# Kernel tuning notes

Hardware: AMD Instinct MI355X
Metric: run time of the kernel (lower is better)

## Reference

```python
import jax, jax.numpy as jnp
import numpy as np

NUM_GRAPHS = 256
NEG_SLOPE = 0.2


def _gatv2(x, src, dst, Wl, Wr, att, bias, num_nodes):
    # GATv2Conv (heads=1): e_ij = att . leaky_relu(Wl x_j + Wr x_i), softmax over in-edges of i
    xl = x @ Wl  # [N, H] source transform
    xr = x @ Wr  # [N, H] target transform
    msg = xl[src]                      # [E, H]
    e = jax.nn.leaky_relu(msg + xr[dst], NEG_SLOPE) @ att  # [E]
    # segment softmax over destination node
    e_max = jax.ops.segment_max(e, dst, num_segments=num_nodes)
    e_exp = jnp.exp(e - e_max[dst])
    denom = jax.ops.segment_sum(e_exp, dst, num_segments=num_nodes)
    alpha = e_exp / denom[dst]         # [E]
    out = jax.ops.segment_sum(alpha[:, None] * msg, dst, num_segments=num_nodes)
    return out + bias


def setup_inputs() -> dict:
    key = jax.random.key(0)
    ks = jax.random.split(key, 16)
    N, E, D, H, O = 100000, 1600000, 64, 64, 64
    s = 0.05
    inp = {
        "x": jax.random.normal(ks[0], (N, D), dtype=jnp.float32),
        "edge_index": jax.random.randint(ks[1], (2, E), 0, N, dtype=jnp.int64),
        "batch": jnp.sort(jax.random.randint(ks[2], (N,), 0, NUM_GRAPHS, dtype=jnp.int64)),
        "W1l": jax.random.normal(ks[3], (D, H), dtype=jnp.float32) * s,
        "W1r": jax.random.normal(ks[4], (D, H), dtype=jnp.float32) * s,
        "att1": jax.random.normal(ks[5], (H,), dtype=jnp.float32) * s,
        "b1": jnp.zeros((H,), dtype=jnp.float32),
        "W2": jax.random.normal(ks[6], (H, H), dtype=jnp.float32) * s,
        "att2": jax.random.normal(ks[7], (H,), dtype=jnp.float32) * s,
        "b2": jnp.zeros((H,), dtype=jnp.float32),
        "W3": jax.random.normal(ks[8], (H, H), dtype=jnp.float32) * s,
        "att3": jax.random.normal(ks[9], (H,), dtype=jnp.float32) * s,
        "b3": jnp.zeros((H,), dtype=jnp.float32),
        "Wlin": jax.random.normal(ks[10], (H, O), dtype=jnp.float32) * s,
        "blin": jnp.zeros((O,), dtype=jnp.float32),
    }
    return inp


def reference(x, edge_index, batch, W1l, W1r, att1, b1, W2, att2, b2, W3, att3, b3, Wlin, blin):
    N = x.shape[0]
    # PyG GATv2Conv default add_self_loops=True
    loops = jnp.arange(N, dtype=edge_index.dtype)
    src = jnp.concatenate([edge_index[0], loops])
    dst = jnp.concatenate([edge_index[1], loops])

    h = jax.nn.relu(_gatv2(x, src, dst, W1l, W1r, att1, b1, N))
    h = jax.nn.relu(_gatv2(h, src, dst, W2, W2, att2, b2, N))  # share_weights=True
    h = _gatv2(h, src, dst, W3, W3, att3, b3, N)

    # global mean pool over graphs
    sums = jax.ops.segment_sum(h, batch, num_segments=NUM_GRAPHS)
    cnts = jax.ops.segment_sum(jnp.ones((N,), dtype=h.dtype), batch, num_segments=NUM_GRAPHS)
    pooled = sums / jnp.maximum(cnts, 1.0)[:, None]
    # dropout is identity in eval mode
    return pooled @ Wlin + blin
```

## Files before the change

kernel.cpp:

```cpp
#include <hip/hip_runtime.h>
#include <hip/hip_fp16.h>
#include <math.h>

#define NEG_SLOPE 0.2f
#define NUM_GRAPHS 256
#define LOG2E_F 1.44269504088896f

#define EPB   6656
#define EPT   13
#define BCAP  5120
#define MAXB  392

typedef _Float16 half8 __attribute__((ext_vector_type(8)));
typedef _Float16 f16x2 __attribute__((ext_vector_type(2)));
typedef float f32x4 __attribute__((ext_vector_type(4)));

__device__ __forceinline__ half8 bch8(uint4 u) { return __builtin_bit_cast(half8, u); }
__device__ __forceinline__ f16x2 bc2(unsigned u) { return __builtin_bit_cast(f16x2, u); }

__device__ __forceinline__ float hsum8_bcast(float x) {
    x += __int_as_float(__builtin_amdgcn_update_dpp(0, __float_as_int(x), 0x111, 0xF, 0xF, false));
    x += __int_as_float(__builtin_amdgcn_update_dpp(0, __float_as_int(x), 0x112, 0xF, 0xF, false));
    x += __int_as_float(__builtin_amdgcn_update_dpp(0, __float_as_int(x), 0x114, 0xF, 0xF, false));
    return __int_as_float(__builtin_amdgcn_ds_swizzle(__float_as_int(x), 0xF8));
}


__device__ __forceinline__ void bucketA_body(char* smem, int bid, int t,
                                             const int* __restrict__ src,
                                             const int* __restrict__ dst,
                                             unsigned* __restrict__ bucketFill,
                                             uint2* __restrict__ bucketArr,
                                             int E, int NBUCK) {
    uint2* sEdge = (uint2*)smem;
    unsigned* hist  = (unsigned*)(smem + EPB * 8);
    unsigned* lscan = hist + MAXB;
    unsigned* ebase = lscan + MAXB;
    unsigned* efill = ebase + MAXB;
    int e0 = bid * EPB;
    int cntE = E - e0; if (cntE > EPB) cntE = EPB;

    for (int b = t; b < MAXB; b += 512) { hist[b] = 0u; efill[b] = 0u; }
    __syncthreads();

    int es[EPT], ed[EPT];
#pragma unroll
    for (int k = 0; k < EPT; ++k) {
        int i = t + k * 512;
        bool v = i < cntE;
        es[k] = v ? src[e0 + i] : 0;
        ed[k] = v ? dst[e0 + i] : -1;
        if (v) atomicAdd(&hist[(unsigned)ed[k] >> 8], 1u);
    }
    __syncthreads();

    if (t < 64) {
        unsigned vals[7]; unsigned tot = 0u;
#pragma unroll
        for (int k = 0; k < 7; ++k) {
            int b = t * 7 + k;
            vals[k] = (b < MAXB) ? hist[b] : 0u;
            tot += vals[k];
        }
        unsigned sc = tot;
#pragma unroll
        for (int off = 1; off < 64; off <<= 1) {
            unsigned n = __shfl_up(sc, off, 64);
            if (t >= off) sc += n;
        }
        unsigned run = sc - tot;
#pragma unroll
        for (int k = 0; k < 7; ++k) {
            int b = t * 7 + k;
            if (b < MAXB) { lscan[b] = run; run += vals[k]; }
        }
    }
    __syncthreads();

    for (int b = t; b < NBUCK; b += 512) {
        unsigned c = hist[b];
        ebase[b] = c ? atomicAdd(&bucketFill[b], c) : 0u;
    }
    __syncthreads();

#pragma unroll
    for (int k = 0; k < EPT; ++k) {
        if (ed[k] >= 0) {
            unsigned b = (unsigned)ed[k] >> 8;
            unsigned p = lscan[b] + atomicAdd(&efill[b], 1u);
            sEdge[p] = make_uint2((unsigned)es[k], (unsigned)ed[k]);
        }
    }
    __syncthreads();

    for (int i = t; i < cntE; i += 512) {
        uint2 e = sEdge[i];
        unsigned b = e.y >> 8;
        unsigned pos = ebase[b] + ((unsigned)i - lscan[b]);
        if (pos < BCAP) bucketArr[(size_t)b * BCAP + pos] = e;
    }
}


__device__ __forceinline__ void stage_x32_row(const float* __restrict__ X, _Float16* sXp,
                                              int r0, int lr, int c0, int N) {
    int row = r0 + lr;
    float4 x0, x1, x2, x3;
    if (row < N) {
        const float4* Xv = (const float4*)(X + (size_t)row * 64 + c0);
        x0 = Xv[0]; x1 = Xv[1]; x2 = Xv[2]; x3 = Xv[3];
    } else {
        x0 = x1 = x2 = x3 = make_float4(0.f, 0.f, 0.f, 0.f);
    }
    __half2 hh[8] = {
        __floats2half2_rn(x0.x, x0.y), __floats2half2_rn(x0.z, x0.w),
        __floats2half2_rn(x1.x, x1.y), __floats2half2_rn(x1.z, x1.w),
        __floats2half2_rn(x2.x, x2.y), __floats2half2_rn(x2.z, x2.w),
        __floats2half2_rn(x3.x, x3.y), __floats2half2_rn(x3.z, x3.w)};
    *(uint4*)(sXp + lr * 72 + c0)     = ((uint4*)hh)[0];
    *(uint4*)(sXp + lr * 72 + c0 + 8) = ((uint4*)hh)[1];
}

__device__ __forceinline__ void stage_x16(const __half* __restrict__ X, _Float16* sXp,
                                          int r0, int t, int N) {
    int lr = t >> 2, c0 = (t & 3) * 16;
    int row = r0 + lr;
    uint4 u0 = make_uint4(0u,0u,0u,0u), u1 = u0;
    if (row < N) {
        const uint4* Xv = (const uint4*)(X + (size_t)row * 64 + c0);
        u0 = Xv[0]; u1 = Xv[1];
    }
    *(uint4*)(sXp + lr * 72 + c0)     = u0;
    *(uint4*)(sXp + lr * 72 + c0 + 8) = u1;
}

__device__ __forceinline__ void stage_wt(const float* __restrict__ W, _Float16* sWt, int t) {
    int k = t >> 2, nq = (t & 3) * 16;
    const float4* wr = (const float4*)(W + k * 64 + nq);
    float4 w0 = wr[0], w1 = wr[1], w2 = wr[2], w3 = wr[3];
    float ws[16] = {w0.x, w0.y, w0.z, w0.w, w1.x, w1.y, w1.z, w1.w,
                    w2.x, w2.y, w2.z, w2.w, w3.x, w3.y, w3.z, w3.w};
#pragma unroll
    for (int i = 0; i < 16; ++i)
        sWt[(nq + i) * 72 + k] = (_Float16)ws[i];
}

__device__ __forceinline__ void stage_wt512(const float* __restrict__ W, _Float16* sWt, int t) {
    int k = t >> 3, nq = (t & 7) * 8;
    const float4* wr = (const float4*)(W + k * 64 + nq);
    float4 w0 = wr[0], w1 = wr[1];
    float ws[8] = {w0.x, w0.y, w0.z, w0.w, w1.x, w1.y, w1.z, w1.w};
#pragma unroll
    for (int i = 0; i < 8; ++i)
        sWt[(nq + i) * 72 + k] = (_Float16)ws[i];
}

__device__ __forceinline__ void mfma_tile(const _Float16* sXp, const _Float16* sWt,
                                          int m0, int lane, f32x4 acc[4]) {
    int lrow = lane & 15, hi = lane >> 4;
    uint4 ua0 = *(const uint4*)(sXp + (m0 + lrow) * 72 + hi * 8);
    uint4 ua1 = *(const uint4*)(sXp + (m0 + lrow) * 72 + 32 + hi * 8);
    half8 a0 = bch8(ua0), a1 = bch8(ua1);
#pragma unroll
    for (int nt = 0; nt < 4; ++nt) {
        uint4 ub0 = *(const uint4*)(sWt + (nt * 16 + lrow) * 72 + hi * 8);
        uint4 ub1 = *(const uint4*)(sWt + (nt * 16 + lrow) * 72 + 32 + hi * 8);
        acc[nt] = __builtin_amdgcn_mfma_f32_16x16x32_f16(a0, bch8(ub0), acc[nt], 0, 0, 0);
        acc[nt] = __builtin_amdgcn_mfma_f32_16x16x32_f16(a1, bch8(ub1), acc[nt], 0, 0, 0);
    }
}

__device__ __forceinline__ void mfma_store_co(const f32x4 acc[4], __half* Y16,
                                              _Float16* srow, int r0, int m0,
                                              int lane, int N) {
    int lrow = lane & 15, hi = lane >> 4;
#pragma unroll
    for (int nt = 0; nt < 4; ++nt)
#pragma unroll
        for (int r = 0; r < 4; ++r)
            srow[(hi * 4 + r) * 72 + nt * 16 + lrow] = (_Float16)acc[nt][r];
    __syncthreads();
    int row = lane >> 3, c8 = (lane & 7) * 8;
#pragma unroll
    for (int i = 0; i < 2; ++i) {
        int m = r0 + m0 + row + i * 8;
        uint4 v = *(const uint4*)(srow + (row + i * 8) * 72 + c8);
        if (m < N) *(uint4*)(Y16 + (size_t)m * 64 + c8) = v;
    }
}

__global__ __launch_bounds__(512) void k_gemm1_bucketA(
        const float* __restrict__ X, const float* __restrict__ Wl, const float* __restrict__ Wr,
        __half* __restrict__ Yl16, __half* __restrict__ Yr16, int N,
        const int* __restrict__ src, const int* __restrict__ dst,
        unsigned* __restrict__ bucketFill, uint2* __restrict__ bucketArr,
        int E, int NBUCK, int aBlocks, int g1Blocks,
        const float* __restrict__ att1, const float* __restrict__ att2,
        const float* __restrict__ att3, __half* __restrict__ att16) {
    __shared__ uint4 smemq[3720];
    char* smem = (char*)smemq;
    int bid = blockIdx.x;
    int t = threadIdx.x;
    if (bid < aBlocks) {
        bucketA_body(smem, bid, t, src, dst, bucketFill, bucketArr, E, NBUCK);
        return;
    }
    if (bid >= aBlocks + g1Blocks) {
        if (t < 192) {
            int layer = t >> 6, f = t & 63;
            const float* ap = (layer == 0) ? att1 : (layer == 1) ? att2 : att3;
            att16[layer * 64 + f] = __float2half(ap[f] * LOG2E_F);
        }
        return;
    }
    _Float16* sXp  = (_Float16*)smem;
    _Float16* sWtl = sXp + 128 * 72;
    _Float16* sWtr = sWtl + 64 * 72;
    _Float16* srep = sWtr + 64 * 72;
    int r0 = (bid - aBlocks) * 128;
    stage_x32_row(X, sXp, r0, t >> 2, (t & 3) * 16, N);
    stage_wt512(Wl, sWtl, t);
    stage_wt512(Wr, sWtr, t);
    __syncthreads();
    int lane = t & 63;
    int m0 = (t >> 6) * 16;
    _Float16* srow = srep + (t >> 6) * 16 * 72;
    f32x4 accl[4] = {}, accr[4] = {};
    mfma_tile(sXp, sWtl, m0, lane, accl);
    mfma_tile(sXp, sWtr, m0, lane, accr);
    mfma_store_co(accl, Yl16, srow, r0, m0, lane, N);
    mfma_store_co(accr, Yr16, srow, r0, m0, lane, N);
}

__global__ __launch_bounds__(512) void k_bucketB(const uint2* __restrict__ bucketArr,
                                                 const unsigned* __restrict__ bucketFill,
                                                 int* __restrict__ cnt, int* __restrict__ csrF,
                                                 const int* __restrict__ batch,
                                                 int* __restrict__ gstart,
                                                 int N, int E) {
    __shared__ int stage[256 * 64];
    __shared__ unsigned h[256];
    int t = threadIdx.x;
    int b = blockIdx.x;
    int n0 = b << 8;
    if (t < 256) h[t] = 1u;
    {
        uint4* sz = (uint4*)stage;
#pragma unroll
        for (int k = 0; k < 8; ++k) sz[t + k * 512] = make_uint4(0u, 0u, 0u, 0u);
    }
    __syncthreads();
    if (t < 256) stage[t << 6] = n0 + t;
    __syncthreads();

    unsigned ec = bucketFill[b]; if (ec > BCAP) ec = BCAP;
    for (unsigned i = t; i < ec; i += 512) {
        uint2 e = bucketArr[(size_t)b * BCAP + i];
        unsigned v = e.y & 255u;
        unsigned r = atomicAdd(&h[v], 1u);
        if (r < 64u) {
            unsigned pos = (r < 32u) ? (((r & 7u) << 2) + (r >> 3))
                                     : (32u + ((r & 7u) << 2) + ((r >> 3) - 4u));
            stage[(v << 6) + pos] = (int)e.x;
        }
    }
    __syncthreads();

    int node = n0 + t;
    if (t < 256 && node < N) {
        unsigned d = h[t];
        cnt[node] = (int)(d < 64u ? d : 64u);
        int bb = batch[node];
        if (node == 0) {
            for (int g = 0; g <= bb; ++g) gstart[g] = 0;
        } else {
            int pb = batch[node - 1];
            for (int g = pb + 1; g <= bb; ++g) gstart[g] = node;
        }
        if (node == N - 1) {
            for (int g = bb + 1; g <= NUM_GRAPHS; ++g) gstart[g] = N;
        }
    }

    int nrows = N - n0; if (nrows > 256) nrows = 256;
    int total4 = nrows << 4;
    uint4* d4 = (uint4*)(csrF + ((size_t)n0 << 6));
    const uint4* s4 = (const uint4*)stage;
    for (int k = t; k < total4; k += 512) d4[k] = s4[k];
}

__global__ __launch_bounds__(256) void k_gemm_l2(const __half* __restrict__ X,
                                                 const float* __restrict__ W,
                                                 __half* __restrict__ Y16, int N) {
    __shared__ _Float16 s[64 * 72 + 64 * 72 + 4 * 16 * 72];
    _Float16* sXp = s;
    _Float16* sWt = s + 64 * 72;
    _Float16* srep = sWt + 64 * 72;
    int t = threadIdx.x;
    int r0 = blockIdx.x * 64;
    stage_x16(X, sXp, r0, t, N);
    stage_wt(W, sWt, t);
    __syncthreads();
    int lane = t & 63;
    int m0 = (t >> 6) * 16;
    _Float16* srow = srep + (t >> 6) * 16 * 72;
    f32x4 acc[4] = {};
    mfma_tile(sXp, sWt, m0, lane, acc);
    mfma_store_co(acc, Y16, srow, r0, m0, lane, N);
}


#define AGG_STEP(P, K)                                                       \
    { half8 v_ = bch8(P);                                                    \
      half8 t_ = v_ + X8;                                                    \
      t_ = __builtin_elementwise_max(t_, t_ * (_Float16)NEG_SLOPE);          \
      uint4 tu_ = __builtin_bit_cast(uint4, t_);                             \
      float sc_ = __builtin_amdgcn_fdot2(bc2(ua.x), bc2(tu_.x), 0.f, false); \
      sc_ = __builtin_amdgcn_fdot2(bc2(ua.y), bc2(tu_.y), sc_, false);       \
      sc_ = __builtin_amdgcn_fdot2(bc2(ua.z), bc2(tu_.z), sc_, false);       \
      sc_ = __builtin_amdgcn_fdot2(bc2(ua.w), bc2(tu_.w), sc_, false);       \
      sc_ = hsum8_bcast(sc_);                                                \
      float w_ = ((K) * 8 + s < degs) ? exp2f(sc_) : 0.f;                    \
      l_acc += w_;                                                           \
      _Pragma("unroll") for (int j_ = 0; j_ < 8; ++j_)                       \
          acc[j_] = fmaf((float)v_[j_], w_, acc[j_]);                        \
    }

__global__ void k_agg8(const __half* __restrict__ xl, const __half* __restrict__ xrh,
                       const __half* __restrict__ att16, const float* __restrict__ bias,
                       const int* __restrict__ cnt, const int* __restrict__ csrF,
                       float* __restrict__ out32, __half* __restrict__ out16,
                       int N, int do_relu) {
    int wid = (blockIdx.x * blockDim.x + threadIdx.x) >> 6;
    if (wid >= N) return;
    int lane = threadIdx.x & 63;
    int q = lane & 7, s = lane >> 3;
    int fb = q * 8;

    int degs = __builtin_amdgcn_readfirstlane(cnt[wid]);
    const int* crow = csrF + ((size_t)wid << 6);

    uint4 idx = *(const uint4*)(crow + s * 4);
    uint4 ux = *(const uint4*)(xrh + ((size_t)wid << 6) + fb);
    uint4 ua = *(const uint4*)(att16 + fb);

    uint4 pA = *(const uint4*)(xl + ((size_t)idx.x << 6) + fb);
    uint4 pB = *(const uint4*)(xl + ((size_t)idx.y << 6) + fb);
    uint4 pC = *(const uint4*)(xl + ((size_t)idx.z << 6) + fb);
    uint4 pD = *(const uint4*)(xl + ((size_t)idx.w << 6) + fb);

    half8 X8 = bch8(ux);
    float l_acc = 0.f;
    float acc[8];
#pragma unroll
    for (int j = 0; j < 8; ++j) acc[j] = 0.f;

    AGG_STEP(pA, 0);
    if (degs > 8)  AGG_STEP(pB, 1);
    if (degs > 16) AGG_STEP(pC, 2);
    if (degs > 24) {
        AGG_STEP(pD, 3);
        if (degs > 32) {
            uint4 idx2 = *(const uint4*)(crow + 32 + s * 4);
            uint4 qA = *(const uint4*)(xl + ((size_t)idx2.x << 6) + fb);
            uint4 qB = *(const uint4*)(xl + ((size_t)idx2.y << 6) + fb);
            uint4 qC = *(const uint4*)(xl + ((size_t)idx2.z << 6) + fb);
            uint4 qD = *(const uint4*)(xl + ((size_t)idx2.w << 6) + fb);
            AGG_STEP(qA, 4);
            if (degs > 40) AGG_STEP(qB, 5);
            if (degs > 48) AGG_STEP(qC, 6);
            if (degs > 56) AGG_STEP(qD, 7);
        }
    }

#pragma unroll
    for (int o = 8; o <= 32; o <<= 1) {
        l_acc += __shfl_xor(l_acc, o, 64);
#pragma unroll
        for (int j = 0; j < 8; ++j) acc[j] += __shfl_xor(acc[j], o, 64);
    }

    if (s < 2) {
        float rl = 1.0f / l_acc;
        float a0 = s ? acc[4] : acc[0];
        float a1 = s ? acc[5] : acc[1];
        float a2 = s ? acc[6] : acc[2];
        float a3 = s ? acc[7] : acc[3];
        int fo = fb + s * 4;
        float4 bv = *(const float4*)(bias + fo);
        a0 = a0 * rl + bv.x; a1 = a1 * rl + bv.y;
        a2 = a2 * rl + bv.z; a3 = a3 * rl + bv.w;
        if (do_relu) {
            a0 = fmaxf(a0, 0.f); a1 = fmaxf(a1, 0.f);
            a2 = fmaxf(a2, 0.f); a3 = fmaxf(a3, 0.f);
        }
        if (out16) {
            __half2 h0 = __floats2half2_rn(a0, a1);
            __half2 h1 = __floats2half2_rn(a2, a3);
            uint2 u;
            u.x = __builtin_bit_cast(unsigned, h0);
            u.y = __builtin_bit_cast(unsigned, h1);
            *(uint2*)(out16 + (size_t)wid * 64 + fo) = u;
        } else {
            *(float4*)(out32 + (size_t)wid * 64 + fo) = make_float4(a0, a1, a2, a3);
        }
    }
}


__global__ __launch_bounds__(256) void k_pool_final(const __half* __restrict__ h16,
                                                    const int* __restrict__ gstart,
                                                    const float* __restrict__ Wlin,
                                                    const float* __restrict__ blin,
                                                    float* __restrict__ out) {
    __shared__ float red[4][64];
    int g = blockIdx.x;
    int t = threadIdx.x;
    int w = t >> 6, lane = t & 63;
    int i0 = gstart[g], i1 = gstart[g + 1];
    const unsigned* hu = (const unsigned*)h16;
    int half_ = lane >> 5;
    int u = lane & 31;
    float sx = 0.f, sy = 0.f;
    for (int i = i0 + w * 2 + half_; i < i1; i += 8) {
        unsigned v = hu[(size_t)i * 32 + u];
        float2 p = __half22float2(__builtin_bit_cast(__half2, v));
        sx += p.x; sy += p.y;
    }
    sx += __shfl_xor(sx, 32, 64);
    sy += __shfl_xor(sy, 32, 64);
    if (lane < 32) { red[w][2 * u] = sx; red[w][2 * u + 1] = sy; }
    __syncthreads();
    if (w == 0) {
        float s = red[0][lane] + red[1][lane] + red[2][lane] + red[3][lane];
        float cden = (float)((i1 - i0) > 1 ? (i1 - i0) : 1);
        float pld = s / cden;
        float acc = blin[lane];
        for (int k = 0; k < 64; ++k) {
            acc += __shfl(pld, k, 64) * Wlin[k * 64 + lane];
        }
        out[g * 64 + lane] = acc;
    }
}


extern "C" void kernel_launch(void* const* d_in, const int* in_sizes, int n_in,
                              void* d_out, int out_size, void* d_ws, size_t ws_size,
                              hipStream_t stream) {
    const float* x    = (const float*)d_in[0];
    const int*   ei   = (const int*)d_in[1];
    const int*   batch= (const int*)d_in[2];
    const float* W1l  = (const float*)d_in[3];
    const float* W1r  = (const float*)d_in[4];
    const float* att1 = (const float*)d_in[5];
    const float* b1   = (const float*)d_in[6];
    const float* W2   = (const float*)d_in[7];
    const float* att2 = (const float*)d_in[8];
    const float* b2   = (const float*)d_in[9];
    const float* W3   = (const float*)d_in[10];
    const float* att3 = (const float*)d_in[11];
    const float* b3   = (const float*)d_in[12];
    const float* Wlin = (const float*)d_in[13];
    const float* blin = (const float*)d_in[14];

    const int N = in_sizes[0] / 64;
    const int E = in_sizes[1] / 2;
    const int* src = ei;
    const int* dst = ei + E;
    const int NBUCK = (N + 255) >> 8;

    char* p = (char*)d_ws;
    auto alloc = [&](size_t bytes) -> void* {
        void* r = (void*)p;
        p += (bytes + 255) & ~(size_t)255;
        return r;
    };
    float*  bufB32 = (float*)alloc((size_t)N * 64 * 4);
    __half* buf16  = (__half*)alloc((size_t)N * 64 * 2);
    __half* bufC16 = (__half*)alloc((size_t)N * 64 * 2);
    int*    csrF   = (int*)alloc((size_t)N * 64 * 4);
    int*    cnt    = (int*)alloc((size_t)N * 4);
    int*    gstart = (int*)alloc((size_t)(NUM_GRAPHS + 1) * 4);
    __half* att16  = (__half*)alloc((size_t)3 * 64 * 2);
    uint2*    bucketArr  = (uint2*)bufB32;
    unsigned* bucketFill = (unsigned*)((char*)bufB32 + ((size_t)20 << 20));

    const int B = 256;
    const int gemmBlocks = (N + 63) / 64;
    const int aggBlocks = ((size_t)N * 64 + B - 1) / B;
    const int aBlocks = (E + EPB - 1) / EPB;
    const int g1Blocks = (N + 127) >> 7;

    hipMemsetAsync(bucketFill, 0, (size_t)NBUCK * 4, stream);
    k_gemm1_bucketA<<<aBlocks + g1Blocks + 1, 512, 0, stream>>>(
        x, W1l, W1r, buf16, bufC16, N, src, dst, bucketFill, bucketArr,
        E, NBUCK, aBlocks, g1Blocks, att1, att2, att3, att16);
    k_bucketB<<<NBUCK, 512, 0, stream>>>(bucketArr, bucketFill, cnt, csrF, batch, gstart, N, E);

    k_agg8<<<aggBlocks, B, 0, stream>>>(buf16, bufC16, att16, b1, cnt, csrF,
                                        nullptr, bufC16, N, 1);
    k_gemm_l2<<<gemmBlocks, B, 0, stream>>>(bufC16, W2, buf16, N);
    k_agg8<<<aggBlocks, B, 0, stream>>>(buf16, buf16, att16 + 64, b2, cnt, csrF,
                                        nullptr, bufC16, N, 1);
    k_gemm_l2<<<gemmBlocks, B, 0, stream>>>(bufC16, W3, buf16, N);
    k_agg8<<<aggBlocks, B, 0, stream>>>(buf16, buf16, att16 + 128, b3, cnt, csrF,
                                        nullptr, bufC16, N, 0);

    k_pool_final<<<NUM_GRAPHS, B, 0, stream>>>(bufC16, gstart, Wlin, blin, (float*)d_out);
}
```

Before: 293.3 us.

## Use nontemporal loads/stores, 128-row GEMM tiles, and trimmed agg reduction

```diff
diff --git a/kernel.cpp b/kernel.cpp
--- a/kernel.cpp
+++ b/kernel.cpp
@@ -14,8 +14,11 @@
 typedef _Float16 half8 __attribute__((ext_vector_type(8)));
 typedef _Float16 f16x2 __attribute__((ext_vector_type(2)));
 typedef float f32x4 __attribute__((ext_vector_type(4)));
+typedef unsigned u32x2 __attribute__((ext_vector_type(2)));
+typedef unsigned u32x4 __attribute__((ext_vector_type(4)));
 
 __device__ __forceinline__ half8 bch8(uint4 u) { return __builtin_bit_cast(half8, u); }
+__device__ __forceinline__ half8 bch8v(u32x4 u) { return __builtin_bit_cast(half8, u); }
 __device__ __forceinline__ f16x2 bc2(unsigned u) { return __builtin_bit_cast(f16x2, u); }
 
 __device__ __forceinline__ float hsum8_bcast(float x) {
@@ -48,8 +51,8 @@
     for (int k = 0; k < EPT; ++k) {
         int i = t + k * 512;
         bool v = i < cntE;
-        es[k] = v ? src[e0 + i] : 0;
-        ed[k] = v ? dst[e0 + i] : -1;
+        es[k] = v ? __builtin_nontemporal_load(src + e0 + i) : 0;
+        ed[k] = v ? __builtin_nontemporal_load(dst + e0 + i) : -1;
         if (v) atomicAdd(&hist[(unsigned)ed[k] >> 8], 1u);
     }
     __syncthreads();
@@ -97,7 +100,10 @@
         uint2 e = sEdge[i];
         unsigned b = e.y >> 8;
         unsigned pos = ebase[b] + ((unsigned)i - lscan[b]);
-        if (pos < BCAP) bucketArr[(size_t)b * BCAP + pos] = e;
+        if (pos < BCAP) {
+            u32x2 pe; pe[0] = e.x; pe[1] = e.y;
+            __builtin_nontemporal_store(pe, (u32x2*)&bucketArr[(size_t)b * BCAP + pos]);
+        }
     }
 }
 
@@ -105,18 +111,19 @@
 __device__ __forceinline__ void stage_x32_row(const float* __restrict__ X, _Float16* sXp,
                                               int r0, int lr, int c0, int N) {
     int row = r0 + lr;
-    float4 x0, x1, x2, x3;
+    f32x4 x0 = {0.f,0.f,0.f,0.f}, x1 = x0, x2 = x0, x3 = x0;
     if (row < N) {
-        const float4* Xv = (const float4*)(X + (size_t)row * 64 + c0);
-        x0 = Xv[0]; x1 = Xv[1]; x2 = Xv[2]; x3 = Xv[3];
-    } else {
-        x0 = x1 = x2 = x3 = make_float4(0.f, 0.f, 0.f, 0.f);
+        const f32x4* Xv = (const f32x4*)(X + (size_t)row * 64 + c0);
+        x0 = __builtin_nontemporal_load(Xv);
+        x1 = __builtin_nontemporal_load(Xv + 1);
+        x2 = __builtin_nontemporal_load(Xv + 2);
+        x3 = __builtin_nontemporal_load(Xv + 3);
     }
     __half2 hh[8] = {
-        __floats2half2_rn(x0.x, x0.y), __floats2half2_rn(x0.z, x0.w),
-        __floats2half2_rn(x1.x, x1.y), __floats2half2_rn(x1.z, x1.w),
-        __floats2half2_rn(x2.x, x2.y), __floats2half2_rn(x2.z, x2.w),
-        __floats2half2_rn(x3.x, x3.y), __floats2half2_rn(x3.z, x3.w)};
+        __floats2half2_rn(x0[0], x0[1]), __floats2half2_rn(x0[2], x0[3]),
+        __floats2half2_rn(x1[0], x1[1]), __floats2half2_rn(x1[2], x1[3]),
+        __floats2half2_rn(x2[0], x2[1]), __floats2half2_rn(x2[2], x2[3]),
+        __floats2half2_rn(x3[0], x3[1]), __floats2half2_rn(x3[2], x3[3])};
     *(uint4*)(sXp + lr * 72 + c0)     = ((uint4*)hh)[0];
     *(uint4*)(sXp + lr * 72 + c0 + 8) = ((uint4*)hh)[1];
 }
@@ -125,13 +132,14 @@
                                           int r0, int t, int N) {
     int lr = t >> 2, c0 = (t & 3) * 16;
     int row = r0 + lr;
-    uint4 u0 = make_uint4(0u,0u,0u,0u), u1 = u0;
+    u32x4 u0 = {0u,0u,0u,0u}, u1 = u0;
     if (row < N) {
-        const uint4* Xv = (const uint4*)(X + (size_t)row * 64 + c0);
-        u0 = Xv[0]; u1 = Xv[1];
-    }
-    *(uint4*)(sXp + lr * 72 + c0)     = u0;
-    *(uint4*)(sXp + lr * 72 + c0 + 8) = u1;
+        const u32x4* Xv = (const u32x4*)(X + (size_t)row * 64 + c0);
+        u0 = __builtin_nontemporal_load(Xv);
+        u1 = __builtin_nontemporal_load(Xv + 1);
+    }
+    *(u32x4*)(sXp + lr * 72 + c0)     = u0;
+    *(u32x4*)(sXp + lr * 72 + c0 + 8) = u1;
 }
 
 __device__ __forceinline__ void stage_wt(const float* __restrict__ W, _Float16* sWt, int t) {
@@ -255,13 +263,13 @@
 
     unsigned ec = bucketFill[b]; if (ec > BCAP) ec = BCAP;
     for (unsigned i = t; i < ec; i += 512) {
-        uint2 e = bucketArr[(size_t)b * BCAP + i];
-        unsigned v = e.y & 255u;
+        u32x2 e = __builtin_nontemporal_load((const u32x2*)&bucketArr[(size_t)b * BCAP + i]);
+        unsigned v = e[1] & 255u;
         unsigned r = atomicAdd(&h[v], 1u);
         if (r < 64u) {
             unsigned pos = (r < 32u) ? (((r & 7u) << 2) + (r >> 3))
                                      : (32u + ((r & 7u) << 2) + ((r >> 3) - 4u));
-            stage[(v << 6) + pos] = (int)e.x;
+            stage[(v << 6) + pos] = (int)e[0];
         }
     }
     __syncthreads();
@@ -292,21 +300,26 @@
 __global__ __launch_bounds__(256) void k_gemm_l2(const __half* __restrict__ X,
                                                  const float* __restrict__ W,
                                                  __half* __restrict__ Y16, int N) {
-    __shared__ _Float16 s[64 * 72 + 64 * 72 + 4 * 16 * 72];
+    __shared__ _Float16 s[128 * 72 + 64 * 72 + 4 * 16 * 72];
     _Float16* sXp = s;
-    _Float16* sWt = s + 64 * 72;
+    _Float16* sWt = s + 128 * 72;
     _Float16* srep = sWt + 64 * 72;
     int t = threadIdx.x;
-    int r0 = blockIdx.x * 64;
+    int r0 = blockIdx.x * 128;
     stage_x16(X, sXp, r0, t, N);
+    stage_x16(X, sXp + 64 * 72, r0 + 64, t, N);
     stage_wt(W, sWt, t);
     __syncthreads();
     int lane = t & 63;
-    int m0 = (t >> 6) * 16;
-    _Float16* srow = srep + (t >> 6) * 16 * 72;
-    f32x4 acc[4] = {};
-    mfma_tile(sXp, sWt, m0, lane, acc);
-    mfma_store_co(acc, Y16, srow, r0, m0, lane, N);
+    int w = t >> 6;
+    _Float16* srow = srep + w * 16 * 72;
+#pragma unroll
+    for (int half_ = 0; half_ < 2; ++half_) {
+        int m0 = half_ * 64 + w * 16;
+        f32x4 acc[4] = {};
+        mfma_tile(sXp, sWt, m0, lane, acc);
+        mfma_store_co(acc, Y16, srow, r0, m0, lane, N);
+    }
 }
 
 
@@ -329,8 +342,7 @@
 __global__ void k_agg8(const __half* __restrict__ xl, const __half* __restrict__ xrh,
                        const __half* __restrict__ att16, const float* __restrict__ bias,
                        const int* __restrict__ cnt, const int* __restrict__ csrF,
-                       float* __restrict__ out32, __half* __restrict__ out16,
-                       int N, int do_relu) {
+                       __half* __restrict__ out16, int N, int do_relu) {
     int wid = (blockIdx.x * blockDim.x + threadIdx.x) >> 6;
     if (wid >= N) return;
     int lane = threadIdx.x & 63;
@@ -340,14 +352,14 @@
     int degs = __builtin_amdgcn_readfirstlane(cnt[wid]);
     const int* crow = csrF + ((size_t)wid << 6);
 
-    uint4 idx = *(const uint4*)(crow + s * 4);
+    u32x4 idxv = __builtin_nontemporal_load((const u32x4*)(crow + s * 4));
     uint4 ux = *(const uint4*)(xrh + ((size_t)wid << 6) + fb);
     uint4 ua = *(const uint4*)(att16 + fb);
 
-    uint4 pA = *(const uint4*)(xl + ((size_t)idx.x << 6) + fb);
-    uint4 pB = *(const uint4*)(xl + ((size_t)idx.y << 6) + fb);
-    uint4 pC = *(const uint4*)(xl + ((size_t)idx.z << 6) + fb);
-    uint4 pD = *(const uint4*)(xl + ((size_t)idx.w << 6) + fb);
+    uint4 pA = *(const uint4*)(xl + ((size_t)idxv[0] << 6) + fb);
+    uint4 pB = *(const uint4*)(xl + ((size_t)idxv[1] << 6) + fb);
+    uint4 pC = *(const uint4*)(xl + ((size_t)idxv[2] << 6) + fb);
+    uint4 pD = *(const uint4*)(xl + ((size_t)idxv[3] << 6) + fb);
 
     half8 X8 = bch8(ux);
     float l_acc = 0.f;
@@ -361,11 +373,11 @@
     if (degs > 24) {
         AGG_STEP(pD, 3);
         if (degs > 32) {
-            uint4 idx2 = *(const uint4*)(crow + 32 + s * 4);
-            uint4 qA = *(const uint4*)(xl + ((size_t)idx2.x << 6) + fb);
-            uint4 qB = *(const uint4*)(xl + ((size_t)idx2.y << 6) + fb);
-            uint4 qC = *(const uint4*)(xl + ((size_t)idx2.z << 6) + fb);
-            uint4 qD = *(const uint4*)(xl + ((size_t)idx2.w << 6) + fb);
+            u32x4 idx2 = __builtin_nontemporal_load((const u32x4*)(crow + 32 + s * 4));
+            uint4 qA = *(const uint4*)(xl + ((size_t)idx2[0] << 6) + fb);
+            uint4 qB = *(const uint4*)(xl + ((size_t)idx2[1] << 6) + fb);
+            uint4 qC = *(const uint4*)(xl + ((size_t)idx2[2] << 6) + fb);
+            uint4 qD = *(const uint4*)(xl + ((size_t)idx2[3] << 6) + fb);
             AGG_STEP(qA, 4);
             if (degs > 40) AGG_STEP(qB, 5);
             if (degs > 48) AGG_STEP(qC, 6);
@@ -373,37 +385,41 @@
         }
     }
 
-#pragma unroll
-    for (int o = 8; o <= 32; o <<= 1) {
+    l_acc += __shfl_xor(l_acc, 8, 64);
+#pragma unroll
+    for (int j = 0; j < 8; ++j) acc[j] += __shfl_xor(acc[j], 8, 64);
+    int par = s & 1;
+    float b0 = par ? acc[4] : acc[0];
+    float b1 = par ? acc[5] : acc[1];
+    float b2 = par ? acc[6] : acc[2];
+    float b3 = par ? acc[7] : acc[3];
+#pragma unroll
+    for (int o = 16; o <= 32; o <<= 1) {
         l_acc += __shfl_xor(l_acc, o, 64);
-#pragma unroll
-        for (int j = 0; j < 8; ++j) acc[j] += __shfl_xor(acc[j], o, 64);
+        b0 += __shfl_xor(b0, o, 64);
+        b1 += __shfl_xor(b1, o, 64);
+        b2 += __shfl_xor(b2, o, 64);
+        b3 += __shfl_xor(b3, o, 64);
     }
 
     if (s < 2) {
         float rl = 1.0f / l_acc;
-        float a0 = s ? acc[4] : acc[0];
-        float a1 = s ? acc[5] : acc[1];
-        float a2 = s ? acc[6] : acc[2];
-        float a3 = s ? acc[7] : acc[3];
         int fo = fb + s * 4;
         float4 bv = *(const float4*)(bias + fo);
-        a0 = a0 * rl + bv.x; a1 = a1 * rl + bv.y;
-        a2 = a2 * rl + bv.z; a3 = a3 * rl + bv.w;
+        float a0 = b0 * rl + bv.x;
+        float a1 = b1 * rl + bv.y;
+        float a2 = b2 * rl + bv.z;
+        float a3 = b3 * rl + bv.w;
         if (do_relu) {
             a0 = fmaxf(a0, 0.f); a1 = fmaxf(a1, 0.f);
             a2 = fmaxf(a2, 0.f); a3 = fmaxf(a3, 0.f);
         }
-        if (out16) {
-            __half2 h0 = __floats2half2_rn(a0, a1);
-            __half2 h1 = __floats2half2_rn(a2, a3);
-            uint2 u;
-            u.x = __builtin_bit_cast(unsigned, h0);
-            u.y = __builtin_bit_cast(unsigned, h1);
-            *(uint2*)(out16 + (size_t)wid * 64 + fo) = u;
-        } else {
-            *(float4*)(out32 + (size_t)wid * 64 + fo) = make_float4(a0, a1, a2, a3);
-        }
+        __half2 h0 = __floats2half2_rn(a0, a1);
+        __half2 h1 = __floats2half2_rn(a2, a3);
+        u32x2 u;
+        u[0] = __builtin_bit_cast(unsigned, h0);
+        u[1] = __builtin_bit_cast(unsigned, h1);
+        __builtin_nontemporal_store(u, (u32x2*)(out16 + (size_t)wid * 64 + fo));
     }
 }
 
@@ -423,7 +439,7 @@
     int u = lane & 31;
     float sx = 0.f, sy = 0.f;
     for (int i = i0 + w * 2 + half_; i < i1; i += 8) {
-        unsigned v = hu[(size_t)i * 32 + u];
+        unsigned v = __builtin_nontemporal_load(hu + (size_t)i * 32 + u);
         float2 p = __half22float2(__builtin_bit_cast(__half2, v));
         sx += p.x; sy += p.y;
     }
@@ -486,7 +502,7 @@
     unsigned* bucketFill = (unsigned*)((char*)bufB32 + ((size_t)20 << 20));
 
     const int B = 256;
-    const int gemmBlocks = (N + 63) / 64;
+    const int gemmBlocks = (N + 127) >> 7;
     const int aggBlocks = ((size_t)N * 64 + B - 1) / B;
     const int aBlocks = (E + EPB - 1) / EPB;
     const int g1Blocks = (N + 127) >> 7;
@@ -498,13 +514,13 @@
     k_bucketB<<<NBUCK, 512, 0, stream>>>(bucketArr, bucketFill, cnt, csrF, batch, gstart, N, E);
 
     k_agg8<<<aggBlocks, B, 0, stream>>>(buf16, bufC16, att16, b1, cnt, csrF,
-                                        nullptr, bufC16, N, 1);
+                                        bufC16, N, 1);
     k_gemm_l2<<<gemmBlocks, B, 0, stream>>>(bufC16, W2, buf16, N);
     k_agg8<<<aggBlocks, B, 0, stream>>>(buf16, buf16, att16 + 64, b2, cnt, csrF,
-                                        nullptr, bufC16, N, 1);
+                                        bufC16, N, 1);
     k_gemm_l2<<<gemmBlocks, B, 0, stream>>>(bufC16, W3, buf16, N);
     k_agg8<<<aggBlocks, B, 0, stream>>>(buf16, buf16, att16 + 128, b3, cnt, csrF,
-                                        nullptr, bufC16, N, 0);
+                                        bufC16, N, 0);
 
     k_pool_final<<<NUM_GRAPHS, B, 0, stream>>>(bufC16, gstart, Wlin, blin, (float*)d_out);
 }
```

Measured after the change: 311.8 us. 1.06x slower.
